# Optimization experiments

Measured on AMD Instinct MI355X. Metric: run time of the kernel, lower is better.

## Reference

```python
import jax, jax.numpy as jnp
import numpy as np
import math

B, H, S, D = 2, 16, 4096, 64

def setup_inputs() -> dict:
    key = jax.random.key(0)
    kq, kk, kv = jax.random.split(key, 3)
    q = jax.random.normal(kq, (B, H, S, D), dtype=jnp.float32)
    k = jax.random.normal(kk, (B, H, S, D), dtype=jnp.float32)
    v = jax.random.normal(kv, (B, H, S, D), dtype=jnp.float32)
    # causal mask: True above the diagonal means 'masked out' (matches masked_fill_)
    mask = ~jnp.tril(jnp.ones((S, S), dtype=bool))
    return {"q": q, "k": k, "v": v, "mask": mask}

def reference(q, k, v, mask):
    head_dim = q.shape[-1]
    scale = 1.0 / math.sqrt(head_dim)
    # scores: [B, H, S, S] -- same math as the chunked torch loop (chunking is a no-op mathematically)
    scores = jnp.einsum('bhqd,bhkd->bhqk', q, k) * scale
    scores = jnp.where(mask[None, None, :, :], -jnp.inf, scores)
    attn = jax.nn.softmax(scores, axis=-1)
    return jnp.einsum('bhqk,bhkd->bhqd', attn, v)
```

## Files before the change

kernel.cpp:

```cpp
#include <hip/hip_runtime.h>
#include <hip/hip_bf16.h>
#include <math.h>

#define SLEN 4096
#define DH   64
#define KVB  64
#define NHEAD 32
#define QBLK 128
#define NQT   (SLEN / QBLK)
#define TILE_E (KVB * DH)

typedef float  f32x4 __attribute__((ext_vector_type(4)));
typedef short  bf16x8 __attribute__((ext_vector_type(8)));
typedef unsigned short u16x8 __attribute__((ext_vector_type(8)));
typedef unsigned short u16x4 __attribute__((ext_vector_type(4)));
union U8 { u16x8 u; bf16x8 b; };
union U4 { unsigned d[4]; bf16x8 b; };

__device__ inline unsigned short f2bf(float f) {
    return __builtin_bit_cast(unsigned short, __float2bfloat16(f));
}
__device__ inline unsigned pk2(float lo, float hi_) {
    return (unsigned)f2bf(lo) | ((unsigned)f2bf(hi_) << 16);
}

__device__ inline void gload16(const unsigned short* g, unsigned short* l) {
    __builtin_amdgcn_global_load_lds(
        (const __attribute__((address_space(1))) void*)g,
        (__attribute__((address_space(3))) void*)l, 16, 0, 0);
}

extern "C" __global__ __launch_bounds__(512)
void prep_kv(const float* __restrict__ K, const float* __restrict__ V,
             unsigned short* __restrict__ Kb, unsigned short* __restrict__ Vt)
{
    const int tile = blockIdx.x & 63;
    const int head = blockIdx.x >> 6;
    const size_t gbase = (size_t)head * SLEN * DH + (size_t)tile * KVB * DH;
    const size_t tbase = ((size_t)head * 64 + tile) * TILE_E;
    const int tid = threadIdx.x;
    if (blockIdx.y == 0) {
        const int row = tid >> 3, d0 = (tid & 7) * 8;
        const float* src = K + gbase + (size_t)row * DH + d0;
        f32x4 a = *(const f32x4*)src, b = *(const f32x4*)(src + 4);
        u16x8 o;
        #pragma unroll
        for (int j = 0; j < 4; ++j) { o[j] = f2bf(a[j]); o[4 + j] = f2bf(b[j]); }
        *(u16x8*)&Kb[tbase + row * 64 + ((unsigned)d0 ^ ((row & 7) << 3))] = o;
    } else {
        const int kk = tid & 63, d0 = (tid >> 6) * 8;
        const int pos = ((kk >> 5) << 5) | (((kk & 15) >> 2) << 3)
                      | (((kk >> 4) & 1) << 2) | (kk & 3);
        const float* src = V + gbase + (size_t)kk * DH + d0;
        f32x4 a = *(const f32x4*)src, b = *(const f32x4*)(src + 4);
        #pragma unroll
        for (int j = 0; j < 8; ++j) {
            const int d = d0 + j;
            const float x = (j < 4) ? a[j] : b[j - 4];
            Vt[tbase + d * 64 + ((unsigned)pos ^ ((d & 7) << 3))] = f2bf(x);
        }
    }
}

extern "C" __global__ __launch_bounds__(256, 3)
void fa_fwd_v11(const float* __restrict__ Q, float* __restrict__ O,
                const unsigned short* __restrict__ Kb,
                const unsigned short* __restrict__ Vt)
{
    const int tid  = threadIdx.x;
    const int lane = tid & 63;
    const int w    = tid >> 6;
    const int l15  = lane & 15;
    const int l4   = lane >> 4;

    const int bid  = (int)blockIdx.x;
    const int qt   = (NQT - 1) - (bid >> 5);
    const int head = bid & 31;
    const size_t qbase  = (size_t)head * SLEN * DH;
    const size_t kvbase = (size_t)head * 64 * TILE_E;

    __shared__ __align__(16) unsigned short Kl[3][TILE_E];
    __shared__ __align__(16) unsigned short Vl[3][TILE_E];

    const float QSC = 0.125f * 1.44269504088896340736f;

    U8 ones;
    #pragma unroll
    for (int j = 0; j < 8; ++j) ones.u[j] = 0x3F80;

    const unsigned short* ksrc = Kb + kvbase;
    const unsigned short* vsrc = Vt + kvbase;

    const int q0   = qt * QBLK;
    const int ntl  = 2 * qt + 2;
    const int wq0  = q0 + w * 32;
    const int qg0  = wq0 + l15;
    const int qg1  = wq0 + 16 + l15;

    auto stage = [&](int b, int t) {
        const size_t toff = (size_t)t * TILE_E;
        const int ib = w * 2;
        gload16(ksrc + toff + ib * 512 + lane * 8,       &Kl[b][ib * 512]);
        gload16(ksrc + toff + (ib + 1) * 512 + lane * 8, &Kl[b][(ib + 1) * 512]);
        gload16(vsrc + toff + ib * 512 + lane * 8,       &Vl[b][ib * 512]);
        gload16(vsrc + toff + (ib + 1) * 512 + lane * 8, &Vl[b][(ib + 1) * 512]);
    };

    bf16x8 aq0[2], aq1[2];
    {
        const float* qp0 = Q + qbase + (size_t)qg0 * DH + l4 * 8;
        const float* qp1 = Q + qbase + (size_t)qg1 * DH + l4 * 8;
        #pragma unroll
        for (int ch = 0; ch < 2; ++ch) {
            f32x4 f0 = *(const f32x4*)(qp0 + ch * 32);
            f32x4 f1 = *(const f32x4*)(qp0 + ch * 32 + 4);
            U4 u;
            u.d[0] = pk2(f0[0] * QSC, f0[1] * QSC);
            u.d[1] = pk2(f0[2] * QSC, f0[3] * QSC);
            u.d[2] = pk2(f1[0] * QSC, f1[1] * QSC);
            u.d[3] = pk2(f1[2] * QSC, f1[3] * QSC);
            aq0[ch] = u.b;
            f0 = *(const f32x4*)(qp1 + ch * 32);
            f1 = *(const f32x4*)(qp1 + ch * 32 + 4);
            u.d[0] = pk2(f0[0] * QSC, f0[1] * QSC);
            u.d[1] = pk2(f0[2] * QSC, f0[3] * QSC);
            u.d[2] = pk2(f1[0] * QSC, f1[1] * QSC);
            u.d[3] = pk2(f1[2] * QSC, f1[3] * QSC);
            aq1[ch] = u.b;
        }
    }

    f32x4 acc0[4] = {}, acc1[4] = {};
    f32x4 lrow0 = {}, lrow1 = {};

    stage(0, 0);
    stage(1, 1);

    int cb = 0, sb = 2;
    for (int t = 0; t < ntl; ++t) {
        const int k0 = t * KVB;
        if (t + 1 < ntl) asm volatile("s_waitcnt vmcnt(4)" ::: "memory");
        else             asm volatile("s_waitcnt vmcnt(0)" ::: "memory");
        __builtin_amdgcn_s_barrier();

        const bool live1 = (k0 <= wq0 + 31);
        if (live1) {
            const bool live0 = (k0 <= wq0 + 15);
            const unsigned short* Kc = &Kl[cb][0];
            const unsigned short* Vc = &Vl[cb][0];

            __builtin_amdgcn_s_setprio(1);
            f32x4 s0[4], s1[4];
            #pragma unroll
            for (int nt = 0; nt < 4; ++nt) {
                const int row = nt * 16 + l15;
                const unsigned rb = (unsigned)row * 64, sw = (unsigned)((row & 7) << 3);
                U8 ak0, ak1;
                ak0.u = *(const u16x8*)&Kc[rb + ((unsigned)(l4 * 8) ^ sw)];
                ak1.u = *(const u16x8*)&Kc[rb + ((unsigned)(32 + l4 * 8) ^ sw)];
                f32x4 z = {};
                if (live0) {
                    z = __builtin_amdgcn_mfma_f32_16x16x32_bf16(ak0.b, aq0[0], z, 0, 0, 0);
                    s0[nt] = __builtin_amdgcn_mfma_f32_16x16x32_bf16(ak1.b, aq0[1], z, 0, 0, 0);
                }
                f32x4 z1 = {};
                z1 = __builtin_amdgcn_mfma_f32_16x16x32_bf16(ak0.b, aq1[0], z1, 0, 0, 0);
                s1[nt] = __builtin_amdgcn_mfma_f32_16x16x32_bf16(ak1.b, aq1[1], s1[nt] = z1, 0, 0, 0);
            }
            __builtin_amdgcn_s_setprio(0);

            if (live0 && (k0 + KVB - 1 > wq0)) {
                #pragma unroll
                for (int nt = 0; nt < 4; ++nt)
                    #pragma unroll
                    for (int r = 0; r < 4; ++r)
                        if (k0 + nt * 16 + l4 * 4 + r > qg0) s0[nt][r] = -INFINITY;
            }
            if (k0 + KVB - 1 > wq0 + 16) {
                #pragma unroll
                for (int nt = 0; nt < 4; ++nt)
                    #pragma unroll
                    for (int r = 0; r < 4; ++r)
                        if (k0 + nt * 16 + l4 * 4 + r > qg1) s1[nt][r] = -INFINITY;
            }

            U4 u00, u01, u10, u11;
            if (live0) {
                u00.d[0] = pk2(exp2f(s0[0][0]), exp2f(s0[0][1]));
                u00.d[1] = pk2(exp2f(s0[0][2]), exp2f(s0[0][3]));
                u00.d[2] = pk2(exp2f(s0[1][0]), exp2f(s0[1][1]));
                u00.d[3] = pk2(exp2f(s0[1][2]), exp2f(s0[1][3]));
                u01.d[0] = pk2(exp2f(s0[2][0]), exp2f(s0[2][1]));
                u01.d[1] = pk2(exp2f(s0[2][2]), exp2f(s0[2][3]));
                u01.d[2] = pk2(exp2f(s0[3][0]), exp2f(s0[3][1]));
                u01.d[3] = pk2(exp2f(s0[3][2]), exp2f(s0[3][3]));
            }
            u10.d[0] = pk2(exp2f(s1[0][0]), exp2f(s1[0][1]));
            u10.d[1] = pk2(exp2f(s1[0][2]), exp2f(s1[0][3]));
            u10.d[2] = pk2(exp2f(s1[1][0]), exp2f(s1[1][1]));
            u10.d[3] = pk2(exp2f(s1[1][2]), exp2f(s1[1][3]));
            u11.d[0] = pk2(exp2f(s1[2][0]), exp2f(s1[2][1]));
            u11.d[1] = pk2(exp2f(s1[2][2]), exp2f(s1[2][3]));
            u11.d[2] = pk2(exp2f(s1[3][0]), exp2f(s1[3][1]));
            u11.d[3] = pk2(exp2f(s1[3][2]), exp2f(s1[3][3]));

            __builtin_amdgcn_s_setprio(1);
            if (live0) {
                lrow0 = __builtin_amdgcn_mfma_f32_16x16x32_bf16(u00.b, ones.b, lrow0, 0, 0, 0);
                lrow0 = __builtin_amdgcn_mfma_f32_16x16x32_bf16(u01.b, ones.b, lrow0, 0, 0, 0);
            }
            lrow1 = __builtin_amdgcn_mfma_f32_16x16x32_bf16(u10.b, ones.b, lrow1, 0, 0, 0);
            lrow1 = __builtin_amdgcn_mfma_f32_16x16x32_bf16(u11.b, ones.b, lrow1, 0, 0, 0);
            #pragma unroll
            for (int nt = 0; nt < 4; ++nt) {
                const int row = nt * 16 + l15;
                const unsigned rb = (unsigned)row * 64, sw = (unsigned)((row & 7) << 3);
                U8 vb0, vb1;
                vb0.u = *(const u16x8*)&Vc[rb + ((unsigned)(l4 * 8) ^ sw)];
                vb1.u = *(const u16x8*)&Vc[rb + ((unsigned)(32 + l4 * 8) ^ sw)];
                if (live0) {
                    acc0[nt] = __builtin_amdgcn_mfma_f32_16x16x32_bf16(u00.b, vb0.b, acc0[nt], 0, 0, 0);
                    acc0[nt] = __builtin_amdgcn_mfma_f32_16x16x32_bf16(u01.b, vb1.b, acc0[nt], 0, 0, 0);
                }
                acc1[nt] = __builtin_amdgcn_mfma_f32_16x16x32_bf16(u10.b, vb0.b, acc1[nt], 0, 0, 0);
                acc1[nt] = __builtin_amdgcn_mfma_f32_16x16x32_bf16(u11.b, vb1.b, acc1[nt], 0, 0, 0);
            }
            __builtin_amdgcn_s_setprio(0);
        }

        if (t + 2 < ntl) stage(sb, t + 2);
        cb = (cb == 2) ? 0 : cb + 1;
        sb = (sb == 2) ? 0 : sb + 1;
    }

    #pragma unroll
    for (int r = 0; r < 4; ++r) {
        const float inv0 = 1.f / lrow0[r];
        const float inv1 = 1.f / lrow1[r];
        float* op0 = O + qbase + (size_t)(wq0 + l4 * 4 + r) * DH + l15;
        float* op1 = O + qbase + (size_t)(wq0 + 16 + l4 * 4 + r) * DH + l15;
        #pragma unroll
        for (int nt = 0; nt < 4; ++nt) {
            op0[nt * 16] = acc0[nt][r] * inv0;
            op1[nt * 16] = acc1[nt][r] * inv1;
        }
    }
}

#define QBLK4 128
#define KPAD 72
#define NQT4  (SLEN/QBLK4)
#define NPAIR4 (NQT4/2)

extern "C" __global__ __launch_bounds__(256)
void fa_fwd_causal(const float* __restrict__ Q, const float* __restrict__ K,
                   const float* __restrict__ V, float* __restrict__ O)
{
    const int tid  = threadIdx.x;
    const int lane = tid & 63;
    const int w    = tid >> 6;
    const int l15  = lane & 15;
    const int l4   = lane >> 4;

    const int bid  = (int)blockIdx.x;
    const int work = (bid & 7) * (NPAIR4 * NHEAD / 8) + (bid >> 3);
    const int head = work >> 4;
    const int pr   = work & (NPAIR4 - 1);
    const size_t base = (size_t)head * SLEN * DH;

    __shared__ unsigned short Kl[2][KVB * KPAD];
    __shared__ unsigned short Vt[2][DH * KPAD];
    __shared__ unsigned short Plds[4][16 * KPAD];

    const float QSC = 0.125f * 1.44269504088896340736f;
    const int krow = tid >> 2,        kc0 = (tid & 3) * 16;
    const int vd0  = (tid >> 4) * 4,  vk0 = (tid & 15) * 4;

    #pragma unroll 1
    for (int ph = 0; ph < 2; ++ph) {
        const int qt  = ph ? (NQT4 - 1 - pr) : pr;
        const int q0  = qt * QBLK4;
        const int ntl = 2 * qt + 2;
        const int qwave = q0 + w * 32;

        bf16x8 aq[2][2];
        #pragma unroll
        for (int set = 0; set < 2; ++set) {
            const int qr = q0 + w * 32 + set * 16 + l15;
            const float* qp = Q + base + (size_t)qr * DH + l4 * 8;
            #pragma unroll
            for (int ch = 0; ch < 2; ++ch) {
                f32x4 f0 = *(const f32x4*)(qp + ch * 32);
                f32x4 f1 = *(const f32x4*)(qp + ch * 32 + 4);
                U8 u;
                #pragma unroll
                for (int j = 0; j < 4; ++j) { u.u[j] = f2bf(f0[j] * QSC); u.u[4 + j] = f2bf(f1[j] * QSC); }
                aq[set][ch] = u.b;
            }
        }

        f32x4 acc[2][4] = {};
        float mrun[2] = { -INFINITY, -INFINITY };
        float lrun[2] = { 0.f, 0.f };
        f32x4 kreg[4], vreg[4];

        auto g_load = [&](int t) {
            const float* kp = K + base + (size_t)(t * KVB + krow) * DH + kc0;
            #pragma unroll
            for (int i = 0; i < 4; ++i) kreg[i] = *(const f32x4*)(kp + i * 4);
            const float* vp = V + base + (size_t)(t * KVB + vk0) * DH + vd0;
            #pragma unroll
            for (int i = 0; i < 4; ++i) vreg[i] = *(const f32x4*)(vp + (size_t)i * DH);
        };
        auto s_write = [&](int c) {
            unsigned short tmp[16];
            #pragma unroll
            for (int i = 0; i < 4; ++i)
                #pragma unroll
                for (int j = 0; j < 4; ++j) tmp[i * 4 + j] = f2bf(kreg[i][j]);
            unsigned short* kd = &Kl[c][krow * KPAD + kc0];
            *(u16x8*)kd       = *(u16x8*)&tmp[0];
            *(u16x8*)(kd + 8) = *(u16x8*)&tmp[8];
            #pragma unroll
            for (int i = 0; i < 4; ++i) {
                u16x4 pk;
                pk[0] = f2bf(vreg[0][i]); pk[1] = f2bf(vreg[1][i]);
                pk[2] = f2bf(vreg[2][i]); pk[3] = f2bf(vreg[3][i]);
                *(u16x4*)&Vt[c][(vd0 + i) * KPAD + vk0] = pk;
            }
        };

        g_load(0); s_write(0); g_load(1);
        __syncthreads();

        for (int t = 0; t < ntl; ++t) {
            const int c  = t & 1;
            const int k0 = t * KVB;
            if (t + 1 < ntl) { s_write(c ^ 1); if (t + 2 < ntl) g_load(t + 2); }

            if (k0 <= qwave + 31) {
                #pragma unroll
                for (int set = 0; set < 2; ++set) {
                    const int qs0 = qwave + set * 16;
                    if (k0 > qs0 + 15) continue;
                    const int q = qs0 + l15;

                    f32x4 s[4];
                    #pragma unroll
                    for (int nt = 0; nt < 4; ++nt) {
                        U8 ak0, ak1;
                        ak0.u = *(const u16x8*)&Kl[c][(nt*16 + l15) * KPAD + l4*8];
                        ak1.u = *(const u16x8*)&Kl[c][(nt*16 + l15) * KPAD + 32 + l4*8];
                        f32x4 z = {};
                        z = __builtin_amdgcn_mfma_f32_16x16x32_bf16(ak0.b, aq[set][0], z, 0, 0, 0);
                        z = __builtin_amdgcn_mfma_f32_16x16x32_bf16(ak1.b, aq[set][1], z, 0, 0, 0);
                        s[nt] = z;
                    }
                    if (k0 + KVB - 1 > qs0) {
                        #pragma unroll
                        for (int nt = 0; nt < 4; ++nt)
                            #pragma unroll
                            for (int r = 0; r < 4; ++r)
                                if (k0 + nt*16 + l4*4 + r > q) s[nt][r] = -INFINITY;
                    }
                    float mx = s[0][0];
                    #pragma unroll
                    for (int nt = 0; nt < 4; ++nt)
                        #pragma unroll
                        for (int r = 0; r < 4; ++r)
                            if (!(nt == 0 && r == 0)) mx = fmaxf(mx, s[nt][r]);
                    mx = fmaxf(mx, __shfl_xor(mx, 16));
                    mx = fmaxf(mx, __shfl_xor(mx, 32));
                    float mn = fmaxf(mrun[set], mx);
                    float fr = exp2f(mrun[set] - mn);
                    mrun[set] = mn;
                    float p[4][4];
                    float rs = 0.f;
                    #pragma unroll
                    for (int nt = 0; nt < 4; ++nt)
                        #pragma unroll
                        for (int r = 0; r < 4; ++r) {
                            float e = exp2f(s[nt][r] - mn);
                            p[nt][r] = e; rs += e;
                        }
                    rs += __shfl_xor(rs, 16);
                    rs += __shfl_xor(rs, 32);
                    lrun[set] = lrun[set] * fr + rs;

                    unsigned short* Pw = &Plds[w][0];
                    #pragma unroll
                    for (int nt = 0; nt < 4; ++nt) {
                        u16x4 pk;
                        pk[0] = f2bf(p[nt][0]); pk[1] = f2bf(p[nt][1]);
                        pk[2] = f2bf(p[nt][2]); pk[3] = f2bf(p[nt][3]);
                        *(u16x4*)&Pw[l15 * KPAD + nt*16 + l4*4] = pk;
                    }
                    #pragma unroll
                    for (int r = 0; r < 4; ++r) {
                        float frr = __shfl(fr, l4*4 + r);
                        #pragma unroll
                        for (int nt = 0; nt < 4; ++nt) acc[set][nt][r] *= frr;
                    }
                    asm volatile("s_waitcnt lgkmcnt(0)" ::: "memory");
                    __builtin_amdgcn_sched_barrier(0);
                    U8 pa0, pa1;
                    pa0.u = *(const u16x8*)&Pw[l15 * KPAD + l4*8];
                    pa1.u = *(const u16x8*)&Pw[l15 * KPAD + 32 + l4*8];
                    #pragma unroll
                    for (int nt = 0; nt < 4; ++nt) {
                        U8 vb0, vb1;
                        vb0.u = *(const u16x8*)&Vt[c][(nt*16 + l15) * KPAD + l4*8];
                        vb1.u = *(const u16x8*)&Vt[c][(nt*16 + l15) * KPAD + 32 + l4*8];
                        acc[set][nt] = __builtin_amdgcn_mfma_f32_16x16x32_bf16(pa0.b, vb0.b, acc[set][nt], 0, 0, 0);
                        acc[set][nt] = __builtin_amdgcn_mfma_f32_16x16x32_bf16(pa1.b, vb1.b, acc[set][nt], 0, 0, 0);
                    }
                }
            }
            __syncthreads();
        }
        #pragma unroll
        for (int set = 0; set < 2; ++set) {
            float inv = 1.f / lrun[set];
            #pragma unroll
            for (int r = 0; r < 4; ++r) {
                float invr = __shfl(inv, l4*4 + r);
                const int qrow = q0 + w*32 + set*16 + l4*4 + r;
                float* op = O + base + (size_t)qrow * DH + l15;
                #pragma unroll
                for (int nt = 0; nt < 4; ++nt)
                    op[nt*16] = acc[set][nt][r] * invr;
            }
        }
        __syncthreads();
    }
}

extern "C" void kernel_launch(void* const* d_in, const int* in_sizes, int n_in,
                              void* d_out, int out_size, void* d_ws, size_t ws_size,
                              hipStream_t stream) {
    (void)in_sizes; (void)n_in; (void)out_size;
    const float* q = (const float*)d_in[0];
    const float* k = (const float*)d_in[1];
    const float* v = (const float*)d_in[2];
    float* o = (float*)d_out;

    const size_t kv_elems = (size_t)NHEAD * 64 * TILE_E;
    const size_t need = 2 * kv_elems * sizeof(unsigned short);
    if (ws_size >= need) {
        unsigned short* Kb = (unsigned short*)d_ws;
        unsigned short* Vtw = Kb + kv_elems;
        prep_kv<<<dim3(NHEAD * 64, 2), 512, 0, stream>>>(k, v, Kb, Vtw);
        fa_fwd_v11<<<dim3(NQT * NHEAD), 256, 0, stream>>>(q, o, Kb, Vtw);
    } else {
        fa_fwd_causal<<<dim3(NPAIR4 * NHEAD), 256, 0, stream>>>(q, k, v, o);
    }
}
```

Baseline: 130.8 us.

## Load K/V fragments directly from global memory, dropping LDS staging and barriers

Removes the triple-buffered LDS pipeline (global_load_lds, waitcnt, block barrier) and has each wave load its swizzled K/V bf16 fragments directly from global memory into registers. Each wave now iterates only over its own causal tile count instead of the block-wide count. This removes barrier synchronization and LDS footprint, possibly raising occupancy, but quadruples global/L2 traffic per block and loses explicit prefetch overlap, exposing load latency.

```diff
diff --git a/kernel.cpp b/kernel.cpp
--- a/kernel.cpp
+++ b/kernel.cpp
@@ -22,12 +22,6 @@
 }
 __device__ inline unsigned pk2(float lo, float hi_) {
     return (unsigned)f2bf(lo) | ((unsigned)f2bf(hi_) << 16);
-}
-
-__device__ inline void gload16(const unsigned short* g, unsigned short* l) {
-    __builtin_amdgcn_global_load_lds(
-        (const __attribute__((address_space(1))) void*)g,
-        (__attribute__((address_space(3))) void*)l, 16, 0, 0);
 }
 
 extern "C" __global__ __launch_bounds__(512)
@@ -63,7 +57,7 @@
 }
 
 extern "C" __global__ __launch_bounds__(256, 3)
-void fa_fwd_v11(const float* __restrict__ Q, float* __restrict__ O,
+void fa_fwd_v13(const float* __restrict__ Q, float* __restrict__ O,
                 const unsigned short* __restrict__ Kb,
                 const unsigned short* __restrict__ Vt)
 {
@@ -79,9 +73,6 @@
     const size_t qbase  = (size_t)head * SLEN * DH;
     const size_t kvbase = (size_t)head * 64 * TILE_E;
 
-    __shared__ __align__(16) unsigned short Kl[3][TILE_E];
-    __shared__ __align__(16) unsigned short Vl[3][TILE_E];
-
     const float QSC = 0.125f * 1.44269504088896340736f;
 
     U8 ones;
@@ -91,20 +82,14 @@
     const unsigned short* ksrc = Kb + kvbase;
     const unsigned short* vsrc = Vt + kvbase;
 
-    const int q0   = qt * QBLK;
-    const int ntl  = 2 * qt + 2;
-    const int wq0  = q0 + w * 32;
-    const int qg0  = wq0 + l15;
-    const int qg1  = wq0 + 16 + l15;
-
-    auto stage = [&](int b, int t) {
-        const size_t toff = (size_t)t * TILE_E;
-        const int ib = w * 2;
-        gload16(ksrc + toff + ib * 512 + lane * 8,       &Kl[b][ib * 512]);
-        gload16(ksrc + toff + (ib + 1) * 512 + lane * 8, &Kl[b][(ib + 1) * 512]);
-        gload16(vsrc + toff + ib * 512 + lane * 8,       &Vl[b][ib * 512]);
-        gload16(vsrc + toff + (ib + 1) * 512 + lane * 8, &Vl[b][(ib + 1) * 512]);
-    };
+    const int wq0 = qt * QBLK + w * 32;
+    const int qg0 = wq0 + l15;
+    const int qg1 = wq0 + 16 + l15;
+    const int ntl = (wq0 + 31) / KVB + 1;
+
+    const unsigned sw   = (unsigned)((l15 & 7) << 3);
+    const int      offA = l15 * 64 + (int)(((unsigned)(l4 * 8)) ^ sw);
+    const int      offB = l15 * 64 + (int)(((unsigned)(32 + l4 * 8)) ^ sw);
 
     bf16x8 aq0[2], aq1[2];
     {
@@ -133,104 +118,82 @@
     f32x4 acc0[4] = {}, acc1[4] = {};
     f32x4 lrow0 = {}, lrow1 = {};
 
-    stage(0, 0);
-    stage(1, 1);
-
-    int cb = 0, sb = 2;
     for (int t = 0; t < ntl; ++t) {
         const int k0 = t * KVB;
-        if (t + 1 < ntl) asm volatile("s_waitcnt vmcnt(4)" ::: "memory");
-        else             asm volatile("s_waitcnt vmcnt(0)" ::: "memory");
-        __builtin_amdgcn_s_barrier();
-
-        const bool live1 = (k0 <= wq0 + 31);
-        if (live1) {
-            const bool live0 = (k0 <= wq0 + 15);
-            const unsigned short* Kc = &Kl[cb][0];
-            const unsigned short* Vc = &Vl[cb][0];
-
-            __builtin_amdgcn_s_setprio(1);
-            f32x4 s0[4], s1[4];
-            #pragma unroll
-            for (int nt = 0; nt < 4; ++nt) {
-                const int row = nt * 16 + l15;
-                const unsigned rb = (unsigned)row * 64, sw = (unsigned)((row & 7) << 3);
-                U8 ak0, ak1;
-                ak0.u = *(const u16x8*)&Kc[rb + ((unsigned)(l4 * 8) ^ sw)];
-                ak1.u = *(const u16x8*)&Kc[rb + ((unsigned)(32 + l4 * 8) ^ sw)];
-                f32x4 z = {};
-                if (live0) {
-                    z = __builtin_amdgcn_mfma_f32_16x16x32_bf16(ak0.b, aq0[0], z, 0, 0, 0);
-                    s0[nt] = __builtin_amdgcn_mfma_f32_16x16x32_bf16(ak1.b, aq0[1], z, 0, 0, 0);
-                }
-                f32x4 z1 = {};
-                z1 = __builtin_amdgcn_mfma_f32_16x16x32_bf16(ak0.b, aq1[0], z1, 0, 0, 0);
-                s1[nt] = __builtin_amdgcn_mfma_f32_16x16x32_bf16(ak1.b, aq1[1], s1[nt] = z1, 0, 0, 0);
-            }
-            __builtin_amdgcn_s_setprio(0);
-
-            if (live0 && (k0 + KVB - 1 > wq0)) {
-                #pragma unroll
-                for (int nt = 0; nt < 4; ++nt)
-                    #pragma unroll
-                    for (int r = 0; r < 4; ++r)
-                        if (k0 + nt * 16 + l4 * 4 + r > qg0) s0[nt][r] = -INFINITY;
-            }
-            if (k0 + KVB - 1 > wq0 + 16) {
-                #pragma unroll
-                for (int nt = 0; nt < 4; ++nt)
-                    #pragma unroll
-                    for (int r = 0; r < 4; ++r)
-                        if (k0 + nt * 16 + l4 * 4 + r > qg1) s1[nt][r] = -INFINITY;
-            }
-
-            U4 u00, u01, u10, u11;
-            if (live0) {
-                u00.d[0] = pk2(exp2f(s0[0][0]), exp2f(s0[0][1]));
-                u00.d[1] = pk2(exp2f(s0[0][2]), exp2f(s0[0][3]));
-                u00.d[2] = pk2(exp2f(s0[1][0]), exp2f(s0[1][1]));
-                u00.d[3] = pk2(exp2f(s0[1][2]), exp2f(s0[1][3]));
-                u01.d[0] = pk2(exp2f(s0[2][0]), exp2f(s0[2][1]));
-                u01.d[1] = pk2(exp2f(s0[2][2]), exp2f(s0[2][3]));
-                u01.d[2] = pk2(exp2f(s0[3][0]), exp2f(s0[3][1]));
-                u01.d[3] = pk2(exp2f(s0[3][2]), exp2f(s0[3][3]));
-            }
-            u10.d[0] = pk2(exp2f(s1[0][0]), exp2f(s1[0][1]));
-            u10.d[1] = pk2(exp2f(s1[0][2]), exp2f(s1[0][3]));
-            u10.d[2] = pk2(exp2f(s1[1][0]), exp2f(s1[1][1]));
-            u10.d[3] = pk2(exp2f(s1[1][2]), exp2f(s1[1][3]));
-            u11.d[0] = pk2(exp2f(s1[2][0]), exp2f(s1[2][1]));
-            u11.d[1] = pk2(exp2f(s1[2][2]), exp2f(s1[2][3]));
-            u11.d[2] = pk2(exp2f(s1[3][0]), exp2f(s1[3][1]));
-            u11.d[3] = pk2(exp2f(s1[3][2]), exp2f(s1[3][3]));
-
-            __builtin_amdgcn_s_setprio(1);
-            if (live0) {
-                lrow0 = __builtin_amdgcn_mfma_f32_16x16x32_bf16(u00.b, ones.b, lrow0, 0, 0, 0);
-                lrow0 = __builtin_amdgcn_mfma_f32_16x16x32_bf16(u01.b, ones.b, lrow0, 0, 0, 0);
-            }
-            lrow1 = __builtin_amdgcn_mfma_f32_16x16x32_bf16(u10.b, ones.b, lrow1, 0, 0, 0);
-            lrow1 = __builtin_amdgcn_mfma_f32_16x16x32_bf16(u11.b, ones.b, lrow1, 0, 0, 0);
-            #pragma unroll
-            for (int nt = 0; nt < 4; ++nt) {
-                const int row = nt * 16 + l15;
-                const unsigned rb = (unsigned)row * 64, sw = (unsigned)((row & 7) << 3);
-                U8 vb0, vb1;
-                vb0.u = *(const u16x8*)&Vc[rb + ((unsigned)(l4 * 8) ^ sw)];
-                vb1.u = *(const u16x8*)&Vc[rb + ((unsigned)(32 + l4 * 8) ^ sw)];
-                if (live0) {
-                    acc0[nt] = __builtin_amdgcn_mfma_f32_16x16x32_bf16(u00.b, vb0.b, acc0[nt], 0, 0, 0);
-                    acc0[nt] = __builtin_amdgcn_mfma_f32_16x16x32_bf16(u01.b, vb1.b, acc0[nt], 0, 0, 0);
-                }
-                acc1[nt] = __builtin_amdgcn_mfma_f32_16x16x32_bf16(u10.b, vb0.b, acc1[nt], 0, 0, 0);
-                acc1[nt] = __builtin_amdgcn_mfma_f32_16x16x32_bf16(u11.b, vb1.b, acc1[nt], 0, 0, 0);
-            }
-            __builtin_amdgcn_s_setprio(0);
-        }
-
-        if (t + 2 < ntl) stage(sb, t + 2);
-        cb = (cb == 2) ? 0 : cb + 1;
-        sb = (sb == 2) ? 0 : sb + 1;
+        const unsigned short* Kt = ksrc + (size_t)t * TILE_E;
+        const unsigned short* Vv = vsrc + (size_t)t * TILE_E;
+
+        U8 ak[4][2], vb[4][2];
+        #pragma unroll
+        for (int nt = 0; nt < 4; ++nt) {
+            ak[nt][0].u = *(const u16x8*)&Kt[nt * 1024 + offA];
+            ak[nt][1].u = *(const u16x8*)&Kt[nt * 1024 + offB];
+        }
+        #pragma unroll
+        for (int nt = 0; nt < 4; ++nt) {
+            vb[nt][0].u = *(const u16x8*)&Vv[nt * 1024 + offA];
+            vb[nt][1].u = *(const u16x8*)&Vv[nt * 1024 + offB];
+        }
+
+        __builtin_amdgcn_s_setprio(1);
+        f32x4 s0[4], s1[4];
+        #pragma unroll
+        for (int nt = 0; nt < 4; ++nt) {
+            f32x4 z = {};
+            z = __builtin_amdgcn_mfma_f32_16x16x32_bf16(ak[nt][0].b, aq0[0], z, 0, 0, 0);
+            s0[nt] = __builtin_amdgcn_mfma_f32_16x16x32_bf16(ak[nt][1].b, aq0[1], z, 0, 0, 0);
+            f32x4 z1 = {};
+            z1 = __builtin_amdgcn_mfma_f32_16x16x32_bf16(ak[nt][0].b, aq1[0], z1, 0, 0, 0);
+            s1[nt] = __builtin_amdgcn_mfma_f32_16x16x32_bf16(ak[nt][1].b, aq1[1], z1, 0, 0, 0);
+        }
+        __builtin_amdgcn_s_setprio(0);
+
+        if (k0 + KVB - 1 > wq0) {
+            #pragma unroll
+            for (int nt = 0; nt < 4; ++nt)
+                #pragma unroll
+                for (int r = 0; r < 4; ++r)
+                    if (k0 + nt * 16 + l4 * 4 + r > qg0) s0[nt][r] = -INFINITY;
+        }
+        if (k0 + KVB - 1 > wq0 + 16) {
+            #pragma unroll
+            for (int nt = 0; nt < 4; ++nt)
+                #pragma unroll
+                for (int r = 0; r < 4; ++r)
+                    if (k0 + nt * 16 + l4 * 4 + r > qg1) s1[nt][r] = -INFINITY;
+        }
+
+        U4 u00, u01, u10, u11;
+        u00.d[0] = pk2(exp2f(s0[0][0]), exp2f(s0[0][1]));
+        u00.d[1] = pk2(exp2f(s0[0][2]), exp2f(s0[0][3]));
+        u00.d[2] = pk2(exp2f(s0[1][0]), exp2f(s0[1][1]));
+        u00.d[3] = pk2(exp2f(s0[1][2]), exp2f(s0[1][3]));
+        u01.d[0] = pk2(exp2f(s0[2][0]), exp2f(s0[2][1]));
+        u01.d[1] = pk2(exp2f(s0[2][2]), exp2f(s0[2][3]));
+        u01.d[2] = pk2(exp2f(s0[3][0]), exp2f(s0[3][1]));
+        u01.d[3] = pk2(exp2f(s0[3][2]), exp2f(s0[3][3]));
+        u10.d[0] = pk2(exp2f(s1[0][0]), exp2f(s1[0][1]));
+        u10.d[1] = pk2(exp2f(s1[0][2]), exp2f(s1[0][3]));
+        u10.d[2] = pk2(exp2f(s1[1][0]), exp2f(s1[1][1]));
+        u10.d[3] = pk2(exp2f(s1[1][2]), exp2f(s1[1][3]));
+        u11.d[0] = pk2(exp2f(s1[2][0]), exp2f(s1[2][1]));
+        u11.d[1] = pk2(exp2f(s1[2][2]), exp2f(s1[2][3]));
+        u11.d[2] = pk2(exp2f(s1[3][0]), exp2f(s1[3][1]));
+        u11.d[3] = pk2(exp2f(s1[3][2]), exp2f(s1[3][3]));
+
+        __builtin_amdgcn_s_setprio(1);
+        lrow0 = __builtin_amdgcn_mfma_f32_16x16x32_bf16(u00.b, ones.b, lrow0, 0, 0, 0);
+        lrow0 = __builtin_amdgcn_mfma_f32_16x16x32_bf16(u01.b, ones.b, lrow0, 0, 0, 0);
+        lrow1 = __builtin_amdgcn_mfma_f32_16x16x32_bf16(u10.b, ones.b, lrow1, 0, 0, 0);
+        lrow1 = __builtin_amdgcn_mfma_f32_16x16x32_bf16(u11.b, ones.b, lrow1, 0, 0, 0);
+        #pragma unroll
+        for (int nt = 0; nt < 4; ++nt) {
+            acc0[nt] = __builtin_amdgcn_mfma_f32_16x16x32_bf16(u00.b, vb[nt][0].b, acc0[nt], 0, 0, 0);
+            acc0[nt] = __builtin_amdgcn_mfma_f32_16x16x32_bf16(u01.b, vb[nt][1].b, acc0[nt], 0, 0, 0);
+            acc1[nt] = __builtin_amdgcn_mfma_f32_16x16x32_bf16(u10.b, vb[nt][0].b, acc1[nt], 0, 0, 0);
+            acc1[nt] = __builtin_amdgcn_mfma_f32_16x16x32_bf16(u11.b, vb[nt][1].b, acc1[nt], 0, 0, 0);
+        }
+        __builtin_amdgcn_s_setprio(0);
     }
 
     #pragma unroll
@@ -450,7 +413,7 @@
         unsigned short* Kb = (unsigned short*)d_ws;
         unsigned short* Vtw = Kb + kv_elems;
         prep_kv<<<dim3(NHEAD * 64, 2), 512, 0, stream>>>(k, v, Kb, Vtw);
-        fa_fwd_v11<<<dim3(NQT * NHEAD), 256, 0, stream>>>(q, o, Kb, Vtw);
+        fa_fwd_v13<<<dim3(NQT * NHEAD), 256, 0, stream>>>(q, o, Kb, Vtw);
     } else {
         fa_fwd_causal<<<dim3(NPAIR4 * NHEAD), 256, 0, stream>>>(q, k, v, o);
     }
```

Result: slower. 162.7 us (+24.4%).
